# Performance work log

Hardware: AMD Instinct MI355X
Metric: run time of the kernel (lower is better)

Reference implementation:

```python
import jax, jax.numpy as jnp
import numpy as np

N_TOK = 384
VOCAB = 50000
N_POS = 52
WDIM = 512
HDIM = 1024
FEAT_DIM = 3 * 16  # np.repeat([len,start,end],16)


def setup_inputs() -> dict:
    key = jax.random.key(0)
    ks = jax.random.split(key, 10)
    s = 0.02  # init scale
    return {
        "sentence": jax.random.randint(ks[0], (N_TOK,), 0, VOCAB),
        "pos_tags": jax.random.randint(ks[1], (N_TOK,), 0, N_POS),
        "We_wrd": jax.random.normal(ks[2], (VOCAB, WDIM), jnp.float32) * s,
        "We_pos": jax.random.normal(ks[3], (N_POS, WDIM), jnp.float32) * s,
        "W_dan1": jax.random.normal(ks[4], (2 * WDIM, HDIM), jnp.float32) * s,
        "b_dan1": jnp.zeros((HDIM,), jnp.float32),
        "W_dan2": jax.random.normal(ks[5], (HDIM, HDIM), jnp.float32) * s,
        "b_dan2": jnp.zeros((HDIM,), jnp.float32),
        "W_s1": jax.random.normal(ks[6], (HDIM + FEAT_DIM, HDIM), jnp.float32) * s,
        "b_s1": jnp.zeros((HDIM,), jnp.float32),
        "W_s2": jax.random.normal(ks[7], (HDIM, 1), jnp.float32) * s,
        "b_s2": jnp.zeros((1,), jnp.float32),
    }


def reference(sentence, pos_tags, We_wrd, We_pos, W_dan1, b_dan1, W_dan2, b_dan2, W_s1, b_s1, W_s2, b_s2):
    n = sentence.shape[0]
    # per-token embedding: concat(pos, word) as in score() with use_pos=True -> [n, 2*wdim]
    emb = jnp.concatenate([We_pos[pos_tags], We_wrd[sentence]], axis=-1)
    # prefix sums so every span mean is O(1): pref[k] = sum of emb[:k]
    pref = jnp.concatenate([jnp.zeros((1, emb.shape[1]), emb.dtype), jnp.cumsum(emb, axis=0)], axis=0)
    # all spans (i, j) with i <= j, as in the double loop over i..n-1, j..n-1
    i_idx, j_idx = np.triu_indices(n)  # static shapes, S = n(n+1)/2
    i_idx = jnp.asarray(i_idx)
    j_idx = jnp.asarray(j_idx)
    end = j_idx + 1
    length = (end - i_idx).astype(emb.dtype)
    # DAN encoder: mean of span embeddings -> 2 relu layers (config['layer']=2)
    mean = (pref[end] - pref[i_idx]) / length[:, None]            # [S, 2*wdim]
    h = jax.nn.relu(mean @ W_dan1 + b_dan1)                        # [S, hdim]
    h = jax.nn.relu(h @ W_dan2 + b_dan2)                           # [S, hdim]
    # phrase feats: np.repeat([len, start, end], 16) -> [S, 48]
    feats = jnp.repeat(jnp.stack([length, i_idx.astype(emb.dtype), end.astype(emb.dtype)], axis=1), 16, axis=1)
    rep = jnp.concatenate([h, feats], axis=1)                      # [S, hdim+48]
    # Wpscore MLP: Linear(ph_dim+48 -> hdim) + relu, Linear(hdim -> 1)
    h2 = jax.nn.relu(rep @ W_s1 + b_s1)
    scores = (h2 @ W_s2 + b_s2)[:, 0]                              # [S]
    return scores
```

## Files before the change

kernel.cpp:

```cpp
#include <hip/hip_runtime.h>

#define NTOK  384
#define SPANS 73920
#define MTILES 584
#define MPAD  (MTILES * 128)
#define HD    1024
#define BK    32
#define KTS   (HD / BK)

typedef unsigned short u16;
typedef __attribute__((ext_vector_type(8))) short short8;
typedef __attribute__((ext_vector_type(4))) float floatx4;

#define VMCNT_IMM(N) (((N) & 0xF) | (((N) >> 4) << 14) | (0x7 << 4) | (0xF << 8))

__device__ __forceinline__ u16 f2bu(float x) {
  union { float f; unsigned u; } un; un.f = x;
  unsigned r = un.u + 0x7fffu + ((un.u >> 16) & 1u);
  return (u16)(r >> 16);
}

__device__ __forceinline__ void gld_lds16(const void* g, void* l) {
  __builtin_amdgcn_global_load_lds(
      (const __attribute__((address_space(1))) void*)g,
      (__attribute__((address_space(3))) void*)l, 16, 0, 0);
}

__global__ void emb_gather(const int* __restrict__ sent, const int* __restrict__ pos,
                           const float* __restrict__ Wwrd, const float* __restrict__ Wpos,
                           u16* __restrict__ embB) {
  int t = blockIdx.x;
  int c = threadIdx.x;
  int pt = pos[t], st = sent[t];
  #pragma unroll
  for (int u = 0; u < 4; ++u) {
    int col = u * 256 + c;
    float v = (col < 512) ? Wpos[(size_t)pt * 512 + col]
                          : Wwrd[(size_t)st * 512 + (col - 512)];
    embB[(size_t)t * HD + col] = f2bu(v);
  }
}

__global__ void prep_spans(int* __restrict__ spI, int* __restrict__ spE, float* __restrict__ spInv,
                           float* __restrict__ scores, const float* __restrict__ bs2) {
  int rf = blockIdx.x * 256 + threadIdx.x;
  if (rf >= MPAD) return;
  int s = rf < SPANS ? rf : SPANS - 1;
  const int n = NTOK;
  double tn = 2.0 * n + 1.0;
  int i = (int)((tn - sqrt(tn * tn - 8.0 * (double)s)) * 0.5);
  if (i < 0) i = 0;
  if (i > n - 1) i = n - 1;
  #define OFF(ii) (((ii) * (2 * n - (ii) + 1)) / 2)
  while (i + 1 <= n - 1 && OFF(i + 1) <= s) ++i;
  while (i > 0 && OFF(i) > s) --i;
  int j = i + (s - OFF(i));
  #undef OFF
  spI[rf] = i;
  spE[rf] = j + 1;
  spInv[rf] = 1.0f / (float)(j + 1 - i);
  if (rf < SPANS) scores[rf] = bs2[0];
}

__global__ void prep_castT(const float* __restrict__ Wd1, const float* __restrict__ Wd2,
                           const float* __restrict__ Ws1,
                           u16* __restrict__ o1, u16* __restrict__ o2, u16* __restrict__ o3) {
  int b = blockIdx.x;
  int w = b >> 10, rem = b & 1023;
  int tk = rem >> 5, tn = rem & 31;
  const float* src = (w == 0) ? Wd1 : ((w == 1) ? Wd2 : Ws1);
  u16* dst = (w == 0) ? o1 : ((w == 1) ? o2 : o3);
  __shared__ u16 tile[32][33];
  int x = threadIdx.x & 31, y = threadIdx.x >> 5;
  int k0 = tk * 32, n0 = tn * 32;
  for (int yy = 0; yy < 32; yy += 8)
    tile[y + yy][x] = f2bu(src[(size_t)(k0 + y + yy) * HD + n0 + x]);
  __syncthreads();
  for (int yy = 0; yy < 32; yy += 8)
    dst[(size_t)(n0 + y + yy) * HD + k0 + x] = tile[x][y + yy];
}

__global__ void prep_svec(const float* __restrict__ Ws1,
                          float* __restrict__ S0, float* __restrict__ S1v, float* __restrict__ S2v) {
  int c = blockIdx.x * 256 + threadIdx.x;
  if (c >= HD) return;
  float a = 0.f, b = 0.f, d = 0.f;
  for (int r = 0; r < 16; ++r) {
    a += Ws1[(size_t)(1024 + r) * HD + c];
    b += Ws1[(size_t)(1040 + r) * HD + c];
    d += Ws1[(size_t)(1056 + r) * HD + c];
  }
  S0[c] = a; S1v[c] = b; S2v[c] = d;
}

__global__ void yscan(const float* __restrict__ Y, float* __restrict__ Qp) {
  __shared__ float buf[NTOK];
  int c = blockIdx.x;
  int t = threadIdx.x;
  buf[t] = Y[(size_t)t * HD + c];
  __syncthreads();
  #pragma unroll
  for (int off = 1; off < NTOK; off <<= 1) {
    float add = (t >= off) ? buf[t - off] : 0.f;
    __syncthreads();
    buf[t] += add;
    __syncthreads();
  }
  if (t == 0) Qp[c] = 0.f;
  Qp[(size_t)(t + 1) * HD + c] = buf[t];
}

__global__ void expand(const float* __restrict__ Qp, const int* __restrict__ spI,
                       const int* __restrict__ spE, const float* __restrict__ spInv,
                       const float* __restrict__ b1, u16* __restrict__ out) {
  int gid = blockIdx.x * 256 + threadIdx.x;
  int row = gid >> 7;
  int c0 = (gid & 127) << 3;
  int i = spI[row], e = spE[row];
  float inv = spInv[row];
  const float* pe = Qp + (size_t)e * HD + c0;
  const float* pi = Qp + (size_t)i * HD + c0;
  const float* bb = b1 + c0;
  u16 tmp[8];
  #pragma unroll
  for (int u = 0; u < 8; ++u) {
    float v = (pe[u] - pi[u]) * inv + bb[u];
    v = v > 0.f ? v : 0.f;
    tmp[u] = f2bu(v);
  }
  *(uint4*)(out + (size_t)row * HD + c0) = *(const uint4*)tmp;
}

template <int EPI>
__global__ __launch_bounds__(256, 3) void gemm_bt(
    const u16* __restrict__ A, const u16* __restrict__ Bt,
    const float* __restrict__ bias, u16* __restrict__ C, float* __restrict__ Cf,
    const int* __restrict__ spI, const int* __restrict__ spE,
    const float* __restrict__ S0, const float* __restrict__ S1v, const float* __restrict__ S2v,
    const float* __restrict__ Ws2, float* __restrict__ scores) {
  __shared__ u16 As[2][128 * BK];
  __shared__ u16 Bs[2][128 * BK];
  int bx = blockIdx.x;
  int mt, nt;
  if (EPI == 2) {
    nt = bx & 7; mt = bx >> 3;
  } else {
    int xcd = bx & 7, k = bx >> 3;
    nt = k & 7;
    mt = xcd + 8 * (k >> 3);
  }
  int m0 = mt * 128, n0 = nt * 128;
  int t = threadIdx.x, lane = t & 63, wid = t >> 6;
  int wm = wid >> 1, wn = wid & 1;
  int q = lane >> 4, r = lane & 15;

  floatx4 acc[4][4] = {};

  int dsub = (lane & 7) ^ ((lane >> 3) & 7);
  int row0 = wid * 16 + 2 * (lane >> 3) + (dsub >> 2);
  int voff = row0 * HD + (dsub & 3) * 8;
  const u16* gA0 = A  + (size_t)m0 * HD;
  const u16* gB0 = Bt + (size_t)n0 * HD;
  int ldsOff0 = wid * 512;
  int ldsOff1 = 2048 + wid * 512;

  auto stage = [&](int kt, int b) {
    const u16* pa = gA0 + voff + kt * BK;
    const u16* pb = gB0 + voff + kt * BK;
    gld_lds16(pa,                   &As[b][ldsOff0]);
    gld_lds16(pa + (size_t)64 * HD, &As[b][ldsOff1]);
    gld_lds16(pb,                   &Bs[b][ldsOff0]);
    gld_lds16(pb + (size_t)64 * HD, &Bs[b][ldsOff1]);
  };

  int oct = (((r & 1) << 2) + q) ^ ((r >> 1) & 7);
  int aoff[4], boff[4];
  #pragma unroll
  for (int x = 0; x < 4; ++x) {
    aoff[x] = (wm * 32 + x * 8 + (r >> 1)) * 64 + oct * 8;
    boff[x] = (wn * 32 + x * 8 + (r >> 1)) * 64 + oct * 8;
  }

  auto compute = [&](int b) {
    short8 af[4];
    #pragma unroll
    for (int x = 0; x < 4; ++x) af[x] = *(const short8*)(&As[b][aoff[x]]);
    #pragma unroll
    for (int ni = 0; ni < 4; ++ni) {
      short8 bf = *(const short8*)(&Bs[b][boff[ni]]);
      #pragma unroll
      for (int mi = 0; mi < 4; ++mi)
        acc[mi][ni] = __builtin_amdgcn_mfma_f32_16x16x32_bf16(af[mi], bf, acc[mi][ni], 0, 0, 0);
    }
  };

  stage(0, 0);
  #pragma unroll 1
  for (int kt = 0; kt < KTS; ++kt) {
    int cur = kt & 1;
    if (kt < KTS - 1) {
      stage(kt + 1, cur ^ 1);
      __builtin_amdgcn_s_waitcnt(VMCNT_IMM(4));
    } else {
      __builtin_amdgcn_s_waitcnt(VMCNT_IMM(0));
    }
    __builtin_amdgcn_s_barrier();
    compute(cur);
    __builtin_amdgcn_s_barrier();
  }

  if (EPI == 2) {
    #pragma unroll
    for (int mi = 0; mi < 4; ++mi) {
      int rowb = m0 + wm * 64 + mi * 16 + q * 4;
      #pragma unroll
      for (int ni = 0; ni < 4; ++ni) {
        int col = n0 + wn * 64 + ni * 16 + r;
        #pragma unroll
        for (int e = 0; e < 4; ++e)
          Cf[(size_t)(rowb + e) * HD + col] = acc[mi][ni][e];
      }
    }
  } else if (EPI == 0) {
    #pragma unroll
    for (int mi = 0; mi < 4; ++mi) {
      int rowb = m0 + wm * 64 + mi * 16 + q * 4;
      #pragma unroll
      for (int ni = 0; ni < 4; ++ni) {
        int col = n0 + wn * 64 + ni * 16 + r;
        float bcol = bias[col];
        #pragma unroll
        for (int e = 0; e < 4; ++e) {
          float v = acc[mi][ni][e] + bcol;
          v = v > 0.f ? v : 0.f;
          C[(size_t)(rowb + e) * HD + col] = f2bu(v);
        }
      }
    }
  } else {
    float bcol[4], s0c[4], s1c[4], s2c[4], wsc[4];
    #pragma unroll
    for (int ni = 0; ni < 4; ++ni) {
      int col = n0 + wn * 64 + ni * 16 + r;
      bcol[ni] = bias[col]; s0c[ni] = S0[col]; s1c[ni] = S1v[col];
      s2c[ni] = S2v[col];  wsc[ni] = Ws2[col];
    }
    #pragma unroll
    for (int mi = 0; mi < 4; ++mi) {
      int rowb = m0 + wm * 64 + mi * 16 + q * 4;
      #pragma unroll
      for (int e = 0; e < 4; ++e) {
        int row = rowb + e;
        float fi = (float)spI[row];
        float fe = (float)spE[row];
        float fl = fe - fi;
        float p = 0.f;
        #pragma unroll
        for (int ni = 0; ni < 4; ++ni) {
          float v = acc[mi][ni][e] + bcol[ni] + fl * s0c[ni] + fi * s1c[ni] + fe * s2c[ni];
          v = v > 0.f ? v : 0.f;
          p += v * wsc[ni];
        }
        p += __shfl_xor(p, 1);
        p += __shfl_xor(p, 2);
        p += __shfl_xor(p, 4);
        p += __shfl_xor(p, 8);
        if (r == 0 && row < SPANS) atomicAdd(&scores[row], p);
      }
    }
  }
}

extern "C" void kernel_launch(void* const* d_in, const int* in_sizes, int n_in,
                              void* d_out, int out_size, void* d_ws, size_t ws_size,
                              hipStream_t stream) {
  const int*   sent = (const int*)d_in[0];
  const int*   pos  = (const int*)d_in[1];
  const float* Wwrd = (const float*)d_in[2];
  const float* Wpos = (const float*)d_in[3];
  const float* Wd1  = (const float*)d_in[4];
  const float* bd1  = (const float*)d_in[5];
  const float* Wd2  = (const float*)d_in[6];
  const float* bd2  = (const float*)d_in[7];
  const float* Ws1  = (const float*)d_in[8];
  const float* bs1  = (const float*)d_in[9];
  const float* Ws2  = (const float*)d_in[10];
  const float* bs2  = (const float*)d_in[11];
  float* scores = (float*)d_out;

  char* w = (char*)d_ws;
  size_t o = 0;
  auto alloc = [&](size_t bytes) {
    char* p = w + o;
    o = (o + bytes + 255) & ~(size_t)255;
    return p;
  };
  int*   spI   = (int*)  alloc((size_t)MPAD * 4);
  int*   spE   = (int*)  alloc((size_t)MPAD * 4);
  float* spInv = (float*)alloc((size_t)MPAD * 4);
  float* S0    = (float*)alloc(4096);
  float* S1v   = (float*)alloc(4096);
  float* S2v   = (float*)alloc(4096);
  u16*   embB  = (u16*)  alloc((size_t)NTOK * HD * 2);
  float* Ybuf  = (float*)alloc((size_t)NTOK * HD * 4);
  float* Qp    = (float*)alloc((size_t)(NTOK + 1) * HD * 4);
  u16* Wd1t = (u16*)alloc((size_t)HD * HD * 2);
  u16* Wd2t = (u16*)alloc((size_t)HD * HD * 2);
  u16* Ws1t = (u16*)alloc((size_t)HD * HD * 2);
  u16* bufA = (u16*)alloc((size_t)MPAD * HD * 2);
  u16* bufB = (u16*)alloc((size_t)MPAD * HD * 2);

  emb_gather<<<NTOK, 256, 0, stream>>>(sent, pos, Wwrd, Wpos, embB);
  prep_spans<<<(MPAD + 255) / 256, 256, 0, stream>>>(spI, spE, spInv, scores, bs2);
  prep_castT<<<3 * 1024, 256, 0, stream>>>(Wd1, Wd2, Ws1, Wd1t, Wd2t, Ws1t);
  prep_svec <<<4, 256, 0, stream>>>(Ws1, S0, S1v, S2v);

  gemm_bt<2><<<(NTOK / 128) * 8, 256, 0, stream>>>(embB, Wd1t, nullptr, nullptr, Ybuf,
                                                   nullptr, nullptr, nullptr, nullptr, nullptr,
                                                   nullptr, nullptr);
  yscan<<<HD, NTOK, 0, stream>>>(Ybuf, Qp);
  expand<<<MPAD / 2, 256, 0, stream>>>(Qp, spI, spE, spInv, bd1, bufA);

  gemm_bt<0><<<MTILES * 8, 256, 0, stream>>>(bufA, Wd2t, bd2, bufB, nullptr,
                                             nullptr, nullptr, nullptr, nullptr, nullptr,
                                             nullptr, nullptr);
  gemm_bt<1><<<MTILES * 8, 256, 0, stream>>>(bufB, Ws1t, bs1, nullptr, nullptr,
                                             spI, spE, S0, S1v, S2v, Ws2, scores);
}
```

Measured before the change: 592.5 us.

## Use 256x256 tiled 512-thread GEMM with 4-stage LDS pipeline for span layers

Replaces the 128x128, 256-thread GEMM for the two large span-level layers with a new 256x256-tile, 8-wave kernel. The new kernel keeps a 4-slot global-to-LDS ring with loads issued three steps ahead, splits each k-step into two MFMA halves with staged loads and s_setprio around the MFMA bursts, and remaps blocks across XCDs. The aim is to raise arithmetic intensity per loaded byte and hide memory latency better. In exchange it uses more LDS and registers per block, so occupancy is lower, and MPAD is padded to a multiple of 256. The old kernel is kept only for the small first layer, with its signature trimmed.

```diff
diff --git a/kernel.cpp b/kernel.cpp
--- a/kernel.cpp
+++ b/kernel.cpp
@@ -2,11 +2,12 @@
 
 #define NTOK  384
 #define SPANS 73920
-#define MTILES 584
-#define MPAD  (MTILES * 128)
+#define MPAD  74752
 #define HD    1024
 #define BK    32
 #define KTS   (HD / BK)
+#define GRID256 1168
+#define CPX256  (GRID256 / 8)
 
 typedef unsigned short u16;
 typedef __attribute__((ext_vector_type(8))) short short8;
@@ -134,21 +135,11 @@
 template <int EPI>
 __global__ __launch_bounds__(256, 3) void gemm_bt(
     const u16* __restrict__ A, const u16* __restrict__ Bt,
-    const float* __restrict__ bias, u16* __restrict__ C, float* __restrict__ Cf,
-    const int* __restrict__ spI, const int* __restrict__ spE,
-    const float* __restrict__ S0, const float* __restrict__ S1v, const float* __restrict__ S2v,
-    const float* __restrict__ Ws2, float* __restrict__ scores) {
+    const float* __restrict__ bias, u16* __restrict__ C, float* __restrict__ Cf) {
   __shared__ u16 As[2][128 * BK];
   __shared__ u16 Bs[2][128 * BK];
   int bx = blockIdx.x;
-  int mt, nt;
-  if (EPI == 2) {
-    nt = bx & 7; mt = bx >> 3;
-  } else {
-    int xcd = bx & 7, k = bx >> 3;
-    nt = k & 7;
-    mt = xcd + 8 * (k >> 3);
-  }
+  int nt = bx & 7, mt = bx >> 3;
   int m0 = mt * 128, n0 = nt * 128;
   int t = threadIdx.x, lane = t & 63, wid = t >> 6;
   int wm = wid >> 1, wn = wid & 1;
@@ -209,26 +200,119 @@
     __builtin_amdgcn_s_barrier();
   }
 
-  if (EPI == 2) {
-    #pragma unroll
-    for (int mi = 0; mi < 4; ++mi) {
-      int rowb = m0 + wm * 64 + mi * 16 + q * 4;
-      #pragma unroll
-      for (int ni = 0; ni < 4; ++ni) {
-        int col = n0 + wn * 64 + ni * 16 + r;
-        #pragma unroll
-        for (int e = 0; e < 4; ++e)
-          Cf[(size_t)(rowb + e) * HD + col] = acc[mi][ni][e];
-      }
-    }
-  } else if (EPI == 0) {
-    #pragma unroll
-    for (int mi = 0; mi < 4; ++mi) {
-      int rowb = m0 + wm * 64 + mi * 16 + q * 4;
-      #pragma unroll
-      for (int ni = 0; ni < 4; ++ni) {
-        int col = n0 + wn * 64 + ni * 16 + r;
-        float bcol = bias[col];
+  #pragma unroll
+  for (int mi = 0; mi < 4; ++mi) {
+    int rowb = m0 + wm * 64 + mi * 16 + q * 4;
+    #pragma unroll
+    for (int ni = 0; ni < 4; ++ni) {
+      int col = n0 + wn * 64 + ni * 16 + r;
+      #pragma unroll
+      for (int e = 0; e < 4; ++e)
+        Cf[(size_t)(rowb + e) * HD + col] = acc[mi][ni][e];
+    }
+  }
+}
+
+template <int EPI>
+__global__ __launch_bounds__(512, 2) void gemm256(
+    const u16* __restrict__ A, const u16* __restrict__ Bt,
+    const float* __restrict__ bias, u16* __restrict__ C,
+    const int* __restrict__ spI, const int* __restrict__ spE,
+    const float* __restrict__ S0, const float* __restrict__ S1v, const float* __restrict__ S2v,
+    const float* __restrict__ Ws2, float* __restrict__ scores) {
+  __shared__ u16 As[4][8192];
+  __shared__ u16 Bs[4][8192];
+
+  int swz = (blockIdx.x & 7) * CPX256 + (blockIdx.x >> 3);
+  int mt = swz >> 2, nt = swz & 3;
+  int m0 = mt * 256, n0 = nt * 256;
+  int t = threadIdx.x, lane = t & 63, wid = t >> 6;
+  int wm = wid >> 2, wn = wid & 3;
+  int q = lane >> 4, r = lane & 15;
+
+  floatx4 acc[8][4] = {};
+
+  int dsub = (lane & 7) ^ ((lane >> 3) & 7);
+  int row0 = wid * 16 + 2 * (lane >> 3) + (dsub >> 2);
+  int voff = row0 * HD + (dsub & 3) * 8;
+  const u16* gA0 = A  + (size_t)m0 * HD;
+  const u16* gB0 = Bt + (size_t)n0 * HD;
+  int ldsOff0 = wid * 512;
+  int ldsOff1 = 4096 + wid * 512;
+
+  auto stageA = [&](int kt) {
+    int slot = kt & 3;
+    const u16* pa = gA0 + voff + kt * BK;
+    gld_lds16(pa,                    &As[slot][ldsOff0]);
+    gld_lds16(pa + (size_t)128 * HD, &As[slot][ldsOff1]);
+  };
+  auto stageB = [&](int kt) {
+    int slot = kt & 3;
+    const u16* pb = gB0 + voff + kt * BK;
+    gld_lds16(pb,                    &Bs[slot][ldsOff0]);
+    gld_lds16(pb + (size_t)128 * HD, &Bs[slot][ldsOff1]);
+  };
+
+  int oct = (((r & 1) << 2) + q) ^ ((r >> 1) & 7);
+  int aoff[8], boff[4];
+  #pragma unroll
+  for (int x = 0; x < 8; ++x) aoff[x] = (wm * 64 + x * 8 + (r >> 1)) * 64 + oct * 8;
+  #pragma unroll
+  for (int x = 0; x < 4; ++x) boff[x] = (wn * 32 + x * 8 + (r >> 1)) * 64 + oct * 8;
+
+  stageA(0); stageB(0);
+  stageA(1); stageB(1);
+  stageA(2); stageB(2);
+  __builtin_amdgcn_s_waitcnt(VMCNT_IMM(8));
+  __builtin_amdgcn_s_barrier();
+
+  #pragma unroll 1
+  for (int kt = 0; kt < KTS; ++kt) {
+    int slot = kt & 3;
+    const u16* sA = As[slot];
+    const u16* sB = Bs[slot];
+
+    short8 af[4], bf[4];
+    #pragma unroll
+    for (int x = 0; x < 4; ++x) af[x] = *(const short8*)(sA + aoff[x]);
+    #pragma unroll
+    for (int x = 0; x < 4; ++x) bf[x] = *(const short8*)(sB + boff[x]);
+    if (kt + 3 < KTS) stageA(kt + 3);
+    __builtin_amdgcn_s_barrier();
+    __builtin_amdgcn_s_setprio(1);
+    #pragma unroll
+    for (int ni = 0; ni < 4; ++ni)
+      #pragma unroll
+      for (int mi = 0; mi < 4; ++mi)
+        acc[mi][ni] = __builtin_amdgcn_mfma_f32_16x16x32_bf16(af[mi], bf[ni], acc[mi][ni], 0, 0, 0);
+    __builtin_amdgcn_s_setprio(0);
+    __builtin_amdgcn_s_barrier();
+
+    #pragma unroll
+    for (int x = 0; x < 4; ++x) af[x] = *(const short8*)(sA + aoff[4 + x]);
+    if (kt + 3 < KTS) stageB(kt + 3);
+    if (kt < KTS - 3)       __builtin_amdgcn_s_waitcnt(VMCNT_IMM(8));
+    else if (kt == KTS - 3) __builtin_amdgcn_s_waitcnt(VMCNT_IMM(4));
+    else                    __builtin_amdgcn_s_waitcnt(VMCNT_IMM(0));
+    __builtin_amdgcn_s_barrier();
+    __builtin_amdgcn_s_setprio(1);
+    #pragma unroll
+    for (int ni = 0; ni < 4; ++ni)
+      #pragma unroll
+      for (int mi = 0; mi < 4; ++mi)
+        acc[4 + mi][ni] = __builtin_amdgcn_mfma_f32_16x16x32_bf16(af[mi], bf[ni], acc[4 + mi][ni], 0, 0, 0);
+    __builtin_amdgcn_s_setprio(0);
+    __builtin_amdgcn_s_barrier();
+  }
+
+  if (EPI == 0) {
+    #pragma unroll
+    for (int ni = 0; ni < 4; ++ni) {
+      int col = n0 + wn * 64 + ni * 16 + r;
+      float bcol = bias[col];
+      #pragma unroll
+      for (int mi = 0; mi < 8; ++mi) {
+        int rowb = m0 + wm * 128 + mi * 16 + q * 4;
         #pragma unroll
         for (int e = 0; e < 4; ++e) {
           float v = acc[mi][ni][e] + bcol;
@@ -246,8 +330,8 @@
       s2c[ni] = S2v[col];  wsc[ni] = Ws2[col];
     }
     #pragma unroll
-    for (int mi = 0; mi < 4; ++mi) {
-      int rowb = m0 + wm * 64 + mi * 16 + q * 4;
+    for (int mi = 0; mi < 8; ++mi) {
+      int rowb = m0 + wm * 128 + mi * 16 + q * 4;
       #pragma unroll
       for (int e = 0; e < 4; ++e) {
         int row = rowb + e;
@@ -315,15 +399,13 @@
   prep_castT<<<3 * 1024, 256, 0, stream>>>(Wd1, Wd2, Ws1, Wd1t, Wd2t, Ws1t);
   prep_svec <<<4, 256, 0, stream>>>(Ws1, S0, S1v, S2v);
 
-  gemm_bt<2><<<(NTOK / 128) * 8, 256, 0, stream>>>(embB, Wd1t, nullptr, nullptr, Ybuf,
-                                                   nullptr, nullptr, nullptr, nullptr, nullptr,
-                                                   nullptr, nullptr);
+  gemm_bt<2><<<(NTOK / 128) * 8, 256, 0, stream>>>(embB, Wd1t, nullptr, nullptr, Ybuf);
   yscan<<<HD, NTOK, 0, stream>>>(Ybuf, Qp);
   expand<<<MPAD / 2, 256, 0, stream>>>(Qp, spI, spE, spInv, bd1, bufA);
 
-  gemm_bt<0><<<MTILES * 8, 256, 0, stream>>>(bufA, Wd2t, bd2, bufB, nullptr,
-                                             nullptr, nullptr, nullptr, nullptr, nullptr,
-                                             nullptr, nullptr);
-  gemm_bt<1><<<MTILES * 8, 256, 0, stream>>>(bufB, Ws1t, bs1, nullptr, nullptr,
-                                             spI, spE, S0, S1v, S2v, Ws2, scores);
-}
+  gemm256<0><<<GRID256, 512, 0, stream>>>(bufA, Wd2t, bd2, bufB,
+                                          nullptr, nullptr, nullptr, nullptr, nullptr,
+                                          nullptr, nullptr);
+  gemm256<1><<<GRID256, 512, 0, stream>>>(bufB, Ws1t, bs1, nullptr,
+                                          spI, spE, S0, S1v, S2v, Ws2, scores);
+}
```

Result: slower. 668.7 us (+12.9%).

## Load B operand fragments directly from global into registers, bypassing LDS

Applied to the files above, without the earlier changes.

The GEMM kernel stops staging the B tile through shared memory. Each lane now loads its B fragments straight from global memory into registers, double-buffered across two register sets, while A keeps going through LDS. The k-loop is unrolled by two so each buffer pair can alternate, with explicit vmcnt waits and scheduling barriers. This halves LDS use and LDS traffic, which may allow higher occupancy. The cost is more global load instructions, because the four waves sharing a B tile each fetch it separately, and more register pressure.

```diff
diff --git a/kernel.cpp b/kernel.cpp
--- a/kernel.cpp
+++ b/kernel.cpp
@@ -139,7 +139,6 @@
     const float* __restrict__ S0, const float* __restrict__ S1v, const float* __restrict__ S2v,
     const float* __restrict__ Ws2, float* __restrict__ scores) {
   __shared__ u16 As[2][128 * BK];
-  __shared__ u16 Bs[2][128 * BK];
   int bx = blockIdx.x;
   int mt, nt;
   if (EPI == 2) {
@@ -159,53 +158,63 @@
   int dsub = (lane & 7) ^ ((lane >> 3) & 7);
   int row0 = wid * 16 + 2 * (lane >> 3) + (dsub >> 2);
   int voff = row0 * HD + (dsub & 3) * 8;
-  const u16* gA0 = A  + (size_t)m0 * HD;
-  const u16* gB0 = Bt + (size_t)n0 * HD;
+  const u16* gA0 = A + (size_t)m0 * HD;
   int ldsOff0 = wid * 512;
   int ldsOff1 = 2048 + wid * 512;
 
   auto stage = [&](int kt, int b) {
     const u16* pa = gA0 + voff + kt * BK;
-    const u16* pb = gB0 + voff + kt * BK;
     gld_lds16(pa,                   &As[b][ldsOff0]);
     gld_lds16(pa + (size_t)64 * HD, &As[b][ldsOff1]);
-    gld_lds16(pb,                   &Bs[b][ldsOff0]);
-    gld_lds16(pb + (size_t)64 * HD, &Bs[b][ldsOff1]);
   };
 
+  const u16* gBf = Bt + ((size_t)(n0 + wn * 64 + r)) * HD + q * 8;
+  auto loadB = [&](int kt, short8 (&bf)[4]) {
+    #pragma unroll
+    for (int ni = 0; ni < 4; ++ni)
+      bf[ni] = *(const short8*)(gBf + (size_t)ni * 16 * HD + kt * BK);
+  };
+
   int oct = (((r & 1) << 2) + q) ^ ((r >> 1) & 7);
-  int aoff[4], boff[4];
+  int aoff[4];
   #pragma unroll
-  for (int x = 0; x < 4; ++x) {
+  for (int x = 0; x < 4; ++x)
     aoff[x] = (wm * 32 + x * 8 + (r >> 1)) * 64 + oct * 8;
-    boff[x] = (wn * 32 + x * 8 + (r >> 1)) * 64 + oct * 8;
-  }
-
-  auto compute = [&](int b) {
+
+  auto compute = [&](int b, short8 (&bf)[4]) {
     short8 af[4];
     #pragma unroll
     for (int x = 0; x < 4; ++x) af[x] = *(const short8*)(&As[b][aoff[x]]);
     #pragma unroll
-    for (int ni = 0; ni < 4; ++ni) {
-      short8 bf = *(const short8*)(&Bs[b][boff[ni]]);
+    for (int ni = 0; ni < 4; ++ni)
       #pragma unroll
       for (int mi = 0; mi < 4; ++mi)
-        acc[mi][ni] = __builtin_amdgcn_mfma_f32_16x16x32_bf16(af[mi], bf, acc[mi][ni], 0, 0, 0);
-    }
+        acc[mi][ni] = __builtin_amdgcn_mfma_f32_16x16x32_bf16(af[mi], bf[ni], acc[mi][ni], 0, 0, 0);
   };
 
+  short8 bfr0[4], bfr1[4];
   stage(0, 0);
+  loadB(0, bfr0);
   #pragma unroll 1
-  for (int kt = 0; kt < KTS; ++kt) {
-    int cur = kt & 1;
-    if (kt < KTS - 1) {
-      stage(kt + 1, cur ^ 1);
-      __builtin_amdgcn_s_waitcnt(VMCNT_IMM(4));
+  for (int kt = 0; kt < KTS; kt += 2) {
+    stage(kt + 1, 1);
+    loadB(kt + 1, bfr1);
+    __builtin_amdgcn_sched_barrier(0);
+    __builtin_amdgcn_s_waitcnt(VMCNT_IMM(6));
+    __builtin_amdgcn_s_barrier();
+    compute(0, bfr0);
+    __builtin_amdgcn_s_barrier();
+    if (kt + 2 < KTS) {
+      stage(kt + 2, 0);
+      loadB(kt + 2, bfr0);
+      __builtin_amdgcn_sched_barrier(0);
+      __builtin_amdgcn_s_waitcnt(VMCNT_IMM(6));
     } else {
+      __builtin_amdgcn_sched_barrier(0);
       __builtin_amdgcn_s_waitcnt(VMCNT_IMM(0));
     }
     __builtin_amdgcn_s_barrier();
-    compute(cur);
+    compute(1, bfr1);
     __builtin_amdgcn_s_barrier();
   }
 
```

New measurement: 878.4 us. +48.3%, slower.
